# Kernel tuning notes

Hardware: AMD Instinct MI355X
Metric: run time of the kernel (lower is better)

## Reference

```python
import jax, jax.numpy as jnp
import numpy as np
import math

H = 1024          # hidden_size
NH = 16           # num heads
HD = H // NH      # head_dim = 64
ORDER = 2         # torsion_order
RANK = 64         # torsion_rank


def setup_inputs() -> dict:
    key = jax.random.key(0)
    ks = jax.random.split(key, 16)
    B, S = 2, 2048
    std = 0.02
    inp = {
        "hidden_states": jax.random.normal(ks[0], (B, S, H), jnp.float32),
        # projection weights stored [in, out] (equivalent to torch Linear W^T)
        "Wq": jax.random.normal(ks[1], (H, H), jnp.float32) * std,
        "bq": jnp.zeros((H,), jnp.float32),
        "Wk": jax.random.normal(ks[2], (H, H), jnp.float32) * std,
        "bk": jnp.zeros((H,), jnp.float32),
        "Wv": jax.random.normal(ks[3], (H, H), jnp.float32) * std,
        "bv": jnp.zeros((H,), jnp.float32),
        "Wo": jax.random.normal(ks[4], (H, H), jnp.float32) * std,
        "bo": jnp.zeros((H,), jnp.float32),
        "q_torsion_a": jax.random.normal(ks[5], (ORDER, H, RANK), jnp.float32) * 0.01,
        "q_torsion_b": jax.random.normal(ks[6], (ORDER, RANK, H), jnp.float32) * 0.01,
        "k_torsion_a": jax.random.normal(ks[7], (ORDER, H, RANK), jnp.float32) * 0.01,
        "k_torsion_b": jax.random.normal(ks[8], (ORDER, RANK, H), jnp.float32) * 0.01,
        "torsion_coupling": jnp.asarray(0.1, jnp.float32),
    }
    return inp


def _apply_torsion(x, ta, tb, coupling):
    # x: [B,S,H]; ta: [ORDER,H,R]; tb: [ORDER,R,H]
    corr = jnp.zeros_like(x)
    for n in range(ORDER):
        low = jnp.einsum('bsh,hr->bsr', x, ta[n])
        lin = jnp.einsum('bsr,rh->bsh', low, tb[n])
        phase = (2.0 * math.pi * (n + 1)) * lin
        corr = corr + jnp.sin(phase) * lin / (n + 1)
    return x + jax.nn.sigmoid(coupling) * corr


def reference(hidden_states, Wq, bq, Wk, bk, Wv, bv, Wo, bo,
              q_torsion_a, q_torsion_b, k_torsion_a, k_torsion_b,
              torsion_coupling):
    B, S, _ = hidden_states.shape
    q = hidden_states @ Wq + bq
    k = hidden_states @ Wk + bk
    v = hidden_states @ Wv + bv
    q = _apply_torsion(q, q_torsion_a, q_torsion_b, torsion_coupling)
    k = _apply_torsion(k, k_torsion_a, k_torsion_b, torsion_coupling)
    # [B, NH, S, HD]
    q = q.reshape(B, S, NH, HD).transpose(0, 2, 1, 3)
    k = k.reshape(B, S, NH, HD).transpose(0, 2, 1, 3)
    v = v.reshape(B, S, NH, HD).transpose(0, 2, 1, 3)
    scale = HD ** -0.5
    attn = jnp.einsum('bhqd,bhkd->bhqk', q, k) * scale
    attn = jax.nn.softmax(attn, axis=-1)
    out = jnp.einsum('bhqk,bhkd->bhqd', attn, v)
    out = out.transpose(0, 2, 1, 3).reshape(B, S, H)
    return out @ Wo + bo
```

## Files before the change

kernel.cpp:

```cpp
#include <hip/hip_runtime.h>
#include <hip/hip_bf16.h>
#include <cstdint>
#include <cstddef>

typedef __bf16 bf16_t;
typedef __bf16 bf16x8 __attribute__((ext_vector_type(8)));
typedef float f32x4 __attribute__((ext_vector_type(4)));

static __device__ __forceinline__ void st_out(float* p, float v) { *p = v; }
static __device__ __forceinline__ void st_out(bf16_t* p, float v) { *p = (bf16_t)v; }

static __device__ __forceinline__ void async_cp16(const bf16_t* g, bf16_t* l) {
  __builtin_amdgcn_global_load_lds(
      (const __attribute__((address_space(1))) void*)g,
      (__attribute__((address_space(3))) void*)l, 16, 0, 0);
}

__global__ __launch_bounds__(256) void prep(const float* __restrict__ hs, bf16_t* __restrict__ hsb,
                                            const float* __restrict__ Wq, const float* __restrict__ Wk,
                                            const float* __restrict__ Wv, const float* __restrict__ Wo,
                                            bf16_t* __restrict__ BtExt, bf16_t* __restrict__ WoT,
                                            bf16_t* __restrict__ Wqb, bf16_t* __restrict__ Wkb,
                                            const float* __restrict__ qta, const float* __restrict__ kta,
                                            bf16_t* __restrict__ qtaT, bf16_t* __restrict__ ktaT,
                                            const float* __restrict__ qtb, const float* __restrict__ ktb,
                                            bf16_t* __restrict__ qtbT, bf16_t* __restrict__ ktbT,
                                            const float* __restrict__ bq, const float* __restrict__ bk,
                                            const float* __restrict__ bv, float* __restrict__ biasN) {
  __shared__ float tile[32][33];
  const int bid = blockIdx.x, t = threadIdx.x;
  const int tx = t & 31, ty = t >> 5;

  if (bid < 2048) {
    int i = (bid * 256 + t) * 8;
    float4 a = *(const float4*)(hs + i);
    float4 b = *(const float4*)(hs + i + 4);
    union { bf16_t h[8]; uint4 u; } p;
    p.h[0] = (bf16_t)a.x; p.h[1] = (bf16_t)a.y; p.h[2] = (bf16_t)a.z; p.h[3] = (bf16_t)a.w;
    p.h[4] = (bf16_t)b.x; p.h[5] = (bf16_t)b.y; p.h[6] = (bf16_t)b.z; p.h[7] = (bf16_t)b.w;
    *(uint4*)(hsb + i) = p.u;
  } else if (bid < 6144) {
    int r = bid - 2048, z = r >> 10, r10 = r & 1023;
    int bx = (r10 & 31) * 32, by = (r10 >> 5) * 32;
    const float* src = z == 0 ? Wq : z == 1 ? Wk : z == 2 ? Wv : Wo;
    bf16_t* dst = z == 3 ? WoT : BtExt + (size_t)z * 1048576;
    bf16_t* sd = z == 0 ? Wqb : z == 1 ? Wkb : nullptr;
#pragma unroll
    for (int i = 0; i < 4; ++i) {
      float v = src[(size_t)(by + ty + i * 8) * 1024 + bx + tx];
      tile[ty + i * 8][tx] = v;
      if (sd) sd[(size_t)(by + ty + i * 8) * 1024 + bx + tx] = (bf16_t)v;
    }
    __syncthreads();
#pragma unroll
    for (int i = 0; i < 4; ++i)
      dst[(size_t)(bx + ty + i * 8) * 1024 + by + tx] = (bf16_t)tile[tx][ty + i * 8];
  } else if (bid < 6400) {
    int r = bid - 6144, z = r >> 6, r6 = r & 63;
    int bx = (r6 & 1) * 32, by = (r6 >> 1) * 32;
    const float* src = ((z >> 1) ? kta : qta) + (size_t)(z & 1) * 65536;
    bf16_t* dst = ((z >> 1) ? ktaT : qtaT) + (size_t)(z & 1) * 65536;
#pragma unroll
    for (int i = 0; i < 4; ++i)
      tile[ty + i * 8][tx] = src[(size_t)(by + ty + i * 8) * 64 + bx + tx];
    __syncthreads();
#pragma unroll
    for (int i = 0; i < 4; ++i)
      dst[(size_t)(bx + ty + i * 8) * 1024 + by + tx] = (bf16_t)tile[tx][ty + i * 8];
  } else if (bid < 6656) {
    int r = bid - 6400, z = r >> 6, r6 = r & 63;
    int bx = (r6 & 31) * 32, by = (r6 >> 5) * 32;
    const float* src = ((z >> 1) ? ktb : qtb) + (size_t)(z & 1) * 65536;
    bf16_t* dst = ((z >> 1) ? ktbT : qtbT) + (size_t)(z & 1) * 65536;
#pragma unroll
    for (int i = 0; i < 4; ++i)
      tile[ty + i * 8][tx] = src[(size_t)(by + ty + i * 8) * 1024 + bx + tx];
    __syncthreads();
#pragma unroll
    for (int i = 0; i < 4; ++i)
      dst[(size_t)(bx + ty + i * 8) * 64 + by + tx] = (bf16_t)tile[tx][ty + i * 8];
  } else if (bid < 6668) {
    int i = (bid - 6656) * 256 + t;
    biasN[i] = (i < 1024) ? bq[i] : (i < 2048 ? bk[i - 1024] : bv[i - 2048]);
  } else {
    int j = t;
    const float* b = (j < 128) ? bq : bk;
    const float* ta = ((j < 128) ? qta : kta) + (size_t)((j >> 6) & 1) * 65536;
    int rr = j & 63;
    float s = 0.f;
    for (int h = 0; h < 1024; ++h) s += b[h] * ta[(size_t)h * 64 + rr];
    biasN[3072 + j] = s;
  }
}

template <typename OutT>
static __device__ __forceinline__ void gemm_core_async(const bf16_t* __restrict__ A, int lda,
                                                       const bf16_t* __restrict__ Bt, int ldb,
                                                       OutT* __restrict__ C, int ldc,
                                                       const float* __restrict__ bias, int K,
                                                       int bx, int by) {
  __shared__ bf16_t As[128][32];
  __shared__ bf16_t Bs[128][32];
  const int m0 = by * 128, n0 = bx * 128;
  const int t = threadIdx.x, w = t >> 6, lane = t & 63;
  const int wm = (w >> 1) * 64, wn = (w & 1) * 64;
  const int quad = lane >> 4, l16 = lane & 15;
  const int sra = lane >> 2, sca = (lane & 3) * 8;
  const bf16_t* Ag0 = A + (size_t)(m0 + w * 16 + sra) * lda + sca;
  const bf16_t* Ag1 = A + (size_t)(m0 + 64 + w * 16 + sra) * lda + sca;
  const bf16_t* Bg0 = Bt + (size_t)(n0 + w * 16 + sra) * ldb + sca;
  const bf16_t* Bg1 = Bt + (size_t)(n0 + 64 + w * 16 + sra) * ldb + sca;
  bf16_t* la0 = &As[0][0] + w * 512;
  bf16_t* la1 = &As[0][0] + 2048 + w * 512;
  bf16_t* lb0 = &Bs[0][0] + w * 512;
  bf16_t* lb1 = &Bs[0][0] + 2048 + w * 512;

  f32x4 acc[4][4] = {};
  for (int k0 = 0; k0 < K; k0 += 32) {
    __syncthreads();
    async_cp16(Ag0 + k0, la0);
    async_cp16(Ag1 + k0, la1);
    async_cp16(Bg0 + k0, lb0);
    async_cp16(Bg1 + k0, lb1);
    __syncthreads();
    bf16x8 af[4], bfr[4];
#pragma unroll
    for (int i = 0; i < 4; ++i)
      af[i] = *(const bf16x8*)&As[wm + i * 16 + l16][quad * 8];
#pragma unroll
    for (int j = 0; j < 4; ++j)
      bfr[j] = *(const bf16x8*)&Bs[wn + j * 16 + l16][quad * 8];
#pragma unroll
    for (int i = 0; i < 4; ++i)
#pragma unroll
      for (int j = 0; j < 4; ++j)
        acc[i][j] = __builtin_amdgcn_mfma_f32_16x16x32_bf16(af[i], bfr[j], acc[i][j], 0, 0, 0);
  }
#pragma unroll
  for (int i = 0; i < 4; ++i) {
    int row = m0 + wm + i * 16 + quad * 4;
#pragma unroll
    for (int j = 0; j < 4; ++j) {
      int col = n0 + wn + j * 16 + l16;
      float bv = bias ? bias[col] : 0.f;
#pragma unroll
      for (int r = 0; r < 4; ++r)
        st_out(&C[(size_t)(row + r) * ldc + col], acc[i][j][r] + bv);
    }
  }
}

template <typename OutT>
static __device__ __forceinline__ void gemm_core_async64(const bf16_t* __restrict__ A, int lda,
                                                         const bf16_t* __restrict__ Bt, int ldb,
                                                         OutT* __restrict__ C, int ldc,
                                                         const float* __restrict__ bias, int K,
                                                         int bx, int by) {
  __shared__ bf16_t As[64][32];
  __shared__ bf16_t Bs[128][32];
  const int m0 = by * 64, n0 = bx * 128;
  const int t = threadIdx.x, w = t >> 6, lane = t & 63;
  const int wm = (w >> 1) * 32, wn = (w & 1) * 64;
  const int quad = lane >> 4, l16 = lane & 15;
  const int sra = lane >> 2, sca = (lane & 3) * 8;
  const bf16_t* Ag0 = A + (size_t)(m0 + w * 16 + sra) * lda + sca;
  const bf16_t* Bg0 = Bt + (size_t)(n0 + w * 16 + sra) * ldb + sca;
  const bf16_t* Bg1 = Bt + (size_t)(n0 + 64 + w * 16 + sra) * ldb + sca;
  bf16_t* la0 = &As[0][0] + w * 512;
  bf16_t* lb0 = &Bs[0][0] + w * 512;
  bf16_t* lb1 = &Bs[0][0] + 2048 + w * 512;

  f32x4 acc[2][4] = {};
  for (int k0 = 0; k0 < K; k0 += 32) {
    __syncthreads();
    async_cp16(Ag0 + k0, la0);
    async_cp16(Bg0 + k0, lb0);
    async_cp16(Bg1 + k0, lb1);
    __syncthreads();
    bf16x8 af[2], bfr[4];
#pragma unroll
    for (int i = 0; i < 2; ++i)
      af[i] = *(const bf16x8*)&As[wm + i * 16 + l16][quad * 8];
#pragma unroll
    for (int j = 0; j < 4; ++j)
      bfr[j] = *(const bf16x8*)&Bs[wn + j * 16 + l16][quad * 8];
#pragma unroll
    for (int i = 0; i < 2; ++i)
#pragma unroll
      for (int j = 0; j < 4; ++j)
        acc[i][j] = __builtin_amdgcn_mfma_f32_16x16x32_bf16(af[i], bfr[j], acc[i][j], 0, 0, 0);
  }
#pragma unroll
  for (int i = 0; i < 2; ++i) {
    int row = m0 + wm + i * 16 + quad * 4;
#pragma unroll
    for (int j = 0; j < 4; ++j) {
      int col = n0 + wn + j * 16 + l16;
      float bv = bias ? bias[col] : 0.f;
#pragma unroll
      for (int r = 0; r < 4; ++r)
        st_out(&C[(size_t)(row + r) * ldc + col], acc[i][j][r] + bv);
    }
  }
}

__global__ __launch_bounds__(256) void gemm_qkv(const bf16_t* __restrict__ A,
                                                const bf16_t* __restrict__ Bt,
                                                bf16_t* __restrict__ C,
                                                const float* __restrict__ biasN) {
  gemm_core_async<bf16_t>(A, 1024, Bt, 1024, C, 3328, biasN, 1024, blockIdx.x, blockIdx.y);
}

__global__ __launch_bounds__(256) void gemm_out(const bf16_t* __restrict__ A,
                                                const bf16_t* __restrict__ Bt,
                                                float* __restrict__ C,
                                                const float* __restrict__ bo) {
  gemm_core_async64<float>(A, 1024, Bt, 1024, C, 1024, bo, 1024, blockIdx.x, blockIdx.y);
}

__global__ __launch_bounds__(256) void gemm_wta(const bf16_t* __restrict__ qtaT,
                                                const bf16_t* __restrict__ ktaT,
                                                const bf16_t* __restrict__ Wqb,
                                                const bf16_t* __restrict__ Wkb,
                                                bf16_t* __restrict__ BtExt) {
  int z = blockIdx.z;
  gemm_core_async64<bf16_t>(z ? ktaT : qtaT, 1024, z ? Wkb : Wqb, 1024,
                            BtExt + (size_t)(3072 + z * 128) * 1024, 1024,
                            nullptr, 1024, blockIdx.x, blockIdx.y);
}

__global__ __launch_bounds__(256) void lin_torsion_fused(const bf16_t* __restrict__ qtbT,
                                                         const bf16_t* __restrict__ ktbT,
                                                         bf16_t* __restrict__ qkv,
                                                         const float* __restrict__ coupling) {
  __shared__ bf16_t As[128][136];
  __shared__ bf16_t Bs0[128][72];
  __shared__ bf16_t Bs1[128][72];
  const int z = blockIdx.z;
  const bf16_t* Low = qkv + 3072 + z * 128;
  const bf16_t* Tb = z ? ktbT : qtbT;
  bf16_t* X = qkv + z * 1024;

  const int m0 = blockIdx.y * 128, n0 = blockIdx.x * 128;
  const int t = threadIdx.x, w = t >> 6, lane = t & 63;
  const int wm = (w >> 1) * 64, wn = (w & 1) * 64;
  const int quad = lane >> 4, l16 = lane & 15;

  {
    const int sr = t >> 1, sc = (t & 1) * 64;
    const bf16_t* Ag = Low + (size_t)(m0 + sr) * 3328 + sc;
#pragma unroll
    for (int i = 0; i < 8; ++i)
      *(float4*)&As[sr][sc + 8 * i] = *(const float4*)(Ag + 8 * i);
    const int br = t >> 1, bc = (t & 1) * 32;
    const bf16_t* Bg0 = Tb + (size_t)(n0 + br) * 64 + bc;
    const bf16_t* Bg1 = Bg0 + 65536;
#pragma unroll
    for (int i = 0; i < 4; ++i) {
      *(float4*)&Bs0[br][bc + 8 * i] = *(const float4*)(Bg0 + 8 * i);
      *(float4*)&Bs1[br][bc + 8 * i] = *(const float4*)(Bg1 + 8 * i);
    }
  }
  __syncthreads();

  f32x4 acc0[4][4] = {}, acc1[4][4] = {};
#pragma unroll
  for (int ks = 0; ks < 2; ++ks) {
    bf16x8 a0[4], a1[4];
#pragma unroll
    for (int i = 0; i < 4; ++i) {
      a0[i] = *(const bf16x8*)&As[wm + i * 16 + l16][ks * 32 + quad * 8];
      a1[i] = *(const bf16x8*)&As[wm + i * 16 + l16][64 + ks * 32 + quad * 8];
    }
#pragma unroll
    for (int j = 0; j < 4; ++j) {
      bf16x8 b0 = *(const bf16x8*)&Bs0[wn + j * 16 + l16][ks * 32 + quad * 8];
      bf16x8 b1 = *(const bf16x8*)&Bs1[wn + j * 16 + l16][ks * 32 + quad * 8];
#pragma unroll
      for (int i = 0; i < 4; ++i) {
        acc0[i][j] = __builtin_amdgcn_mfma_f32_16x16x32_bf16(a0[i], b0, acc0[i][j], 0, 0, 0);
        acc1[i][j] = __builtin_amdgcn_mfma_f32_16x16x32_bf16(a1[i], b1, acc1[i][j], 0, 0, 0);
      }
    }
  }

  const float PI2 = 6.283185307179586f;
  const float sig = 1.f / (1.f + __expf(-coupling[0]));
  const float scale = z ? 1.f : 0.1803368801111204f;
#pragma unroll
  for (int i = 0; i < 4; ++i) {
#pragma unroll
    for (int j = 0; j < 4; ++j) {
#pragma unroll
      for (int r = 0; r < 4; ++r) {
        int row = m0 + wm + i * 16 + quad * 4 + r;
        int col = n0 + wn + j * 16 + l16;
        size_t idx = (size_t)row * 3328 + col;
        float l1 = acc0[i][j][r], l2 = acc1[i][j][r];
        float corr = __sinf(PI2 * l1) * l1 + __sinf(2.f * PI2 * l2) * l2 * 0.5f;
        X[idx] = (bf16_t)(((float)X[idx] + sig * corr) * scale);
      }
    }
  }
}

__global__ __launch_bounds__(256, 2) void flash_attn(const bf16_t* __restrict__ qkv,
                                                     bf16_t* __restrict__ aout) {
  constexpr int LD = 3328, SEQ = 2048;
  const int qb = blockIdx.x, bh = blockIdx.y;
  const int b = bh >> 4, h = bh & 15;
  const size_t base = (size_t)b * SEQ * LD + h * 64;
  const bf16_t* Qg = qkv + base;
  const bf16_t* Kg = qkv + base + 1024;
  const bf16_t* Vg = qkv + base + 2048;

  __shared__ __align__(16) unsigned char smem[29696];
  bf16_t(*VT)[136] = (bf16_t(*)[136])smem;
  float* LDSo = (float*)smem;
  float* Lred = (float*)(smem + 24576);
  float* invL = (float*)(smem + 28672);

  const int t = threadIdx.x, w = t >> 6, lane = t & 63;
  const int kw = w >> 1, qw = w & 1;
  const int quad = lane >> 4, l16 = lane & 15;
  const int q0 = qb * 128;

  bf16x8 qf[4][2];
  {
    const bf16_t* Qrow = Qg + (size_t)(q0 + qw * 64 + l16) * LD + quad * 8;
#pragma unroll
    for (int nf = 0; nf < 4; ++nf)
#pragma unroll
      for (int ks = 0; ks < 2; ++ks)
        qf[nf][ks] = *(const bf16x8*)(Qrow + (size_t)(nf * 16) * LD + ks * 32);
  }

  f32x4 o[4][4] = {};
  float l_part[4] = {0.f, 0.f, 0.f, 0.f};

  const int vg = t >> 3, vcb = (t & 7) * 8;
  const int colb = (((vg >> 3) << 5) | ((vg & 3) << 3) | (((vg >> 2) & 1) << 2)) ^ ((t & 7) << 3);
  const bf16_t* Vbase = Vg + (size_t)(vg * 4) * LD + vcb;
  const bf16_t* Krow = Kg + (size_t)(kw * 64 + l16) * LD + quad * 8;

  for (int k0 = 0; k0 < SEQ; k0 += 128) {
    __syncthreads();
    {
      const bf16_t* vsrc = Vbase + (size_t)k0 * LD;
      union { float4 f; bf16_t h[8]; } vr[4];
#pragma unroll
      for (int kk = 0; kk < 4; ++kk)
        vr[kk].f = *(const float4*)(vsrc + (size_t)kk * LD);
#pragma unroll
      for (int cc = 0; cc < 8; ++cc) {
        union { bf16_t h[4]; uint2 u; } pk;
#pragma unroll
        for (int kk = 0; kk < 4; ++kk) pk.h[kk] = vr[kk].h[cc];
        *(uint2*)&VT[vcb + cc][colb] = pk.u;
      }
    }
    bf16x8 kf[4][2];
#pragma unroll
    for (int jk = 0; jk < 4; ++jk)
#pragma unroll
      for (int ks = 0; ks < 2; ++ks)
        kf[jk][ks] = *(const bf16x8*)(Krow + (size_t)(k0 + jk * 16) * LD + ks * 32);
    __syncthreads();

    f32x4 st[4][4] = {};
#pragma unroll
    for (int ks = 0; ks < 2; ++ks)
#pragma unroll
      for (int jk = 0; jk < 4; ++jk)
#pragma unroll
        for (int nf = 0; nf < 4; ++nf)
          st[jk][nf] = __builtin_amdgcn_mfma_f32_16x16x32_bf16(kf[jk][ks], qf[nf][ks], st[jk][nf], 0, 0, 0);

    bf16x8 Pp[2][4];
#pragma unroll
    for (int g = 0; g < 2; ++g)
#pragma unroll
      for (int nf = 0; nf < 4; ++nf) {
        union { bf16_t h[8]; bf16x8 v; } ph;
#pragma unroll
        for (int b2 = 0; b2 < 2; ++b2)
#pragma unroll
          for (int r = 0; r < 4; ++r) {
            float p = exp2f(st[g * 2 + b2][nf][r]);
            l_part[nf] += p;
            ph.h[b2 * 4 + r] = (bf16_t)p;
          }
        Pp[g][nf] = ph.v;
      }

#pragma unroll
    for (int g = 0; g < 2; ++g) {
      bf16x8 vf[4];
#pragma unroll
      for (int jd = 0; jd < 4; ++jd) {
        int row = jd * 16 + l16;
        int col = (kw * 64 + g * 32 + quad * 8) ^ ((((row >> 3) & 7)) << 3);
        vf[jd] = *(const bf16x8*)&VT[row][col];
      }
#pragma unroll
      for (int jd = 0; jd < 4; ++jd)
#pragma unroll
        for (int nf = 0; nf < 4; ++nf)
          o[jd][nf] = __builtin_amdgcn_mfma_f32_16x16x32_bf16(vf[jd], Pp[g][nf], o[jd][nf], 0, 0, 0);
    }
  }

  __syncthreads();
#pragma unroll
  for (int nf = 0; nf < 4; ++nf)
    Lred[((kw * 2 + qw) * 4 + quad) * 64 + nf * 16 + l16] = l_part[nf];
  __syncthreads();
  if (t < 128) {
    int qw2 = t >> 6, ql = t & 63;
    float s = 0.f;
#pragma unroll
    for (int kw2 = 0; kw2 < 2; ++kw2)
#pragma unroll
      for (int qd = 0; qd < 4; ++qd)
        s += Lred[((kw2 * 2 + qw2) * 4 + qd) * 64 + ql];
    invL[t] = 1.f / s;
  }
  __syncthreads();

  const int rq = t >> 1, rc0 = (t & 1) * 8;
#pragma unroll
  for (int jd = 0; jd < 4; ++jd) {
#pragma unroll
    for (int nf = 0; nf < 4; ++nf)
      *(f32x4*)&LDSo[(size_t)(kw * 128 + qw * 64 + nf * 16 + l16) * 24 + quad * 4] = o[jd][nf];
    __syncthreads();
    f32x4 a0 = *(const f32x4*)&LDSo[(size_t)rq * 24 + rc0];
    f32x4 a1 = *(const f32x4*)&LDSo[(size_t)(128 + rq) * 24 + rc0];
    f32x4 b0 = *(const f32x4*)&LDSo[(size_t)rq * 24 + rc0 + 4];
    f32x4 b1 = *(const f32x4*)&LDSo[(size_t)(128 + rq) * 24 + rc0 + 4];
    float iv = invL[rq];
    union { bf16_t h[8]; uint4 u; } pk;
#pragma unroll
    for (int r = 0; r < 4; ++r) {
      pk.h[r] = (bf16_t)((a0[r] + a1[r]) * iv);
      pk.h[4 + r] = (bf16_t)((b0[r] + b1[r]) * iv);
    }
    *(uint4*)&aout[(size_t)(b * SEQ + q0 + rq) * 1024 + h * 64 + jd * 16 + rc0] = pk.u;
    if (jd < 3) __syncthreads();
  }
}

extern "C" void kernel_launch(void* const* d_in, const int* in_sizes, int n_in,
                              void* d_out, int out_size, void* d_ws, size_t ws_size,
                              hipStream_t stream) {
  const float* hs   = (const float*)d_in[0];
  const float* Wq   = (const float*)d_in[1];
  const float* bq   = (const float*)d_in[2];
  const float* Wk   = (const float*)d_in[3];
  const float* bk   = (const float*)d_in[4];
  const float* Wv   = (const float*)d_in[5];
  const float* bv   = (const float*)d_in[6];
  const float* Wo   = (const float*)d_in[7];
  const float* bo   = (const float*)d_in[8];
  const float* qta  = (const float*)d_in[9];
  const float* qtb  = (const float*)d_in[10];
  const float* kta  = (const float*)d_in[11];
  const float* ktb  = (const float*)d_in[12];
  const float* coup = (const float*)d_in[13];
  float* out = (float*)d_out;

  uint8_t* ws = (uint8_t*)d_ws;
  bf16_t* hsb   = (bf16_t*)(ws);
  bf16_t* aout  = (bf16_t*)(ws);
  bf16_t* BtExt = (bf16_t*)(ws + 8388608);
  bf16_t* WoT   = (bf16_t*)(ws + 16777216);
  float*  biasN = (float*)(ws + 18874368);
  bf16_t* qkv   = (bf16_t*)(ws + 18890752);
  bf16_t* Wqb   = (bf16_t*)(ws + 46153728);
  bf16_t* Wkb   = (bf16_t*)(ws + 48250880);
  bf16_t* qtaT  = (bf16_t*)(ws + 50348032);
  bf16_t* ktaT  = (bf16_t*)(ws + 50610176);
  bf16_t* qtbT  = (bf16_t*)(ws + 50872320);
  bf16_t* ktbT  = (bf16_t*)(ws + 51134464);

  dim3 b256(256);

  prep<<<6669, b256, 0, stream>>>(hs, hsb, Wq, Wk, Wv, Wo, BtExt, WoT, Wqb, Wkb,
                                  qta, kta, qtaT, ktaT, qtb, ktb, qtbT, ktbT,
                                  bq, bk, bv, biasN);
  gemm_wta<<<dim3(8, 2, 2), b256, 0, stream>>>(qtaT, ktaT, Wqb, Wkb, BtExt);
  gemm_qkv<<<dim3(26, 32), b256, 0, stream>>>(hsb, BtExt, qkv, biasN);
  lin_torsion_fused<<<dim3(8, 32, 2), b256, 0, stream>>>(qtbT, ktbT, qkv, coup);
  flash_attn<<<dim3(16, 32), b256, 0, stream>>>(qkv, aout);
  gemm_out<<<dim3(8, 64), b256, 0, stream>>>(aout, WoT, out, bo);
}
```

Baseline: 290.4 us.

## Double-buffer V tile in LDS and prefetch next K/V in flash attention

```diff
diff --git a/kernel.cpp b/kernel.cpp
--- a/kernel.cpp
+++ b/kernel.cpp
@@ -314,8 +314,9 @@
   const bf16_t* Kg = qkv + base + 1024;
   const bf16_t* Vg = qkv + base + 2048;
 
-  __shared__ __align__(16) unsigned char smem[29696];
-  bf16_t(*VT)[136] = (bf16_t(*)[136])smem;
+  __shared__ __align__(16) unsigned char smem[34816];
+  bf16_t(*VT0)[136] = (bf16_t(*)[136])smem;
+  bf16_t(*VT1)[136] = (bf16_t(*)[136])(smem + 17408);
   float* LDSo = (float*)smem;
   float* Lred = (float*)(smem + 24576);
   float* invL = (float*)(smem + 28672);
@@ -343,31 +344,35 @@
   const bf16_t* Vbase = Vg + (size_t)(vg * 4) * LD + vcb;
   const bf16_t* Krow = Kg + (size_t)(kw * 64 + l16) * LD + quad * 8;
 
+  float4 vr[4];
+  bf16x8 kf[4][2];
+
+#pragma unroll
+  for (int kk = 0; kk < 4; ++kk)
+    vr[kk] = *(const float4*)(Vbase + (size_t)kk * LD);
+#pragma unroll
+  for (int cc = 0; cc < 8; ++cc) {
+    union { bf16_t h[4]; uint2 u; } pk;
+#pragma unroll
+    for (int kk = 0; kk < 4; ++kk) pk.h[kk] = ((const bf16_t*)&vr[kk])[cc];
+    *(uint2*)&VT0[vcb + cc][colb] = pk.u;
+  }
+#pragma unroll
+  for (int kk = 0; kk < 4; ++kk)
+    vr[kk] = *(const float4*)(Vbase + (size_t)(128 + kk) * LD);
+#pragma unroll
+  for (int jk = 0; jk < 4; ++jk)
+#pragma unroll
+    for (int ks = 0; ks < 2; ++ks)
+      kf[jk][ks] = *(const bf16x8*)(Krow + (size_t)(jk * 16) * LD + ks * 32);
+  __syncthreads();
+
   for (int k0 = 0; k0 < SEQ; k0 += 128) {
-    __syncthreads();
-    {
-      const bf16_t* vsrc = Vbase + (size_t)k0 * LD;
-      union { float4 f; bf16_t h[8]; } vr[4];
-#pragma unroll
-      for (int kk = 0; kk < 4; ++kk)
-        vr[kk].f = *(const float4*)(vsrc + (size_t)kk * LD);
-#pragma unroll
-      for (int cc = 0; cc < 8; ++cc) {
-        union { bf16_t h[4]; uint2 u; } pk;
-#pragma unroll
-        for (int kk = 0; kk < 4; ++kk) pk.h[kk] = vr[kk].h[cc];
-        *(uint2*)&VT[vcb + cc][colb] = pk.u;
-      }
-    }
-    bf16x8 kf[4][2];
-#pragma unroll
-    for (int jk = 0; jk < 4; ++jk)
-#pragma unroll
-      for (int ks = 0; ks < 2; ++ks)
-        kf[jk][ks] = *(const bf16x8*)(Krow + (size_t)(k0 + jk * 16) * LD + ks * 32);
-    __syncthreads();
+    bf16_t(*VTc)[136] = ((k0 >> 7) & 1) ? VT1 : VT0;
+    bf16_t(*VTn)[136] = ((k0 >> 7) & 1) ? VT0 : VT1;
 
     f32x4 st[4][4] = {};
+    __builtin_amdgcn_s_setprio(1);
 #pragma unroll
     for (int ks = 0; ks < 2; ++ks)
 #pragma unroll
@@ -375,24 +380,45 @@
 #pragma unroll
         for (int nf = 0; nf < 4; ++nf)
           st[jk][nf] = __builtin_amdgcn_mfma_f32_16x16x32_bf16(kf[jk][ks], qf[nf][ks], st[jk][nf], 0, 0, 0);
+    __builtin_amdgcn_s_setprio(0);
 
     bf16x8 Pp[2][4];
 #pragma unroll
     for (int g = 0; g < 2; ++g)
 #pragma unroll
       for (int nf = 0; nf < 4; ++nf) {
-        union { bf16_t h[8]; bf16x8 v; } ph;
+        union { bf16_t hh[8]; bf16x8 v; } ph;
 #pragma unroll
         for (int b2 = 0; b2 < 2; ++b2)
 #pragma unroll
           for (int r = 0; r < 4; ++r) {
             float p = exp2f(st[g * 2 + b2][nf][r]);
             l_part[nf] += p;
-            ph.h[b2 * 4 + r] = (bf16_t)p;
+            ph.hh[b2 * 4 + r] = (bf16_t)p;
           }
         Pp[g][nf] = ph.v;
       }
 
+    if (k0 + 128 < SEQ) {
+#pragma unroll
+      for (int cc = 0; cc < 8; ++cc) {
+        union { bf16_t h[4]; uint2 u; } pk;
+#pragma unroll
+        for (int kk = 0; kk < 4; ++kk) pk.h[kk] = ((const bf16_t*)&vr[kk])[cc];
+        *(uint2*)&VTn[vcb + cc][colb] = pk.u;
+      }
+      if (k0 + 256 < SEQ) {
+#pragma unroll
+        for (int kk = 0; kk < 4; ++kk)
+          vr[kk] = *(const float4*)(Vbase + (size_t)(k0 + 256 + kk) * LD);
+      }
+#pragma unroll
+      for (int jk = 0; jk < 4; ++jk)
+#pragma unroll
+        for (int ks = 0; ks < 2; ++ks)
+          kf[jk][ks] = *(const bf16x8*)(Krow + (size_t)(k0 + 128 + jk * 16) * LD + ks * 32);
+    }
+
 #pragma unroll
     for (int g = 0; g < 2; ++g) {
       bf16x8 vf[4];
@@ -400,17 +426,20 @@
       for (int jd = 0; jd < 4; ++jd) {
         int row = jd * 16 + l16;
         int col = (kw * 64 + g * 32 + quad * 8) ^ ((((row >> 3) & 7)) << 3);
-        vf[jd] = *(const bf16x8*)&VT[row][col];
+        vf[jd] = *(const bf16x8*)&VTc[row][col];
       }
+      __builtin_amdgcn_s_setprio(1);
 #pragma unroll
       for (int jd = 0; jd < 4; ++jd)
 #pragma unroll
         for (int nf = 0; nf < 4; ++nf)
           o[jd][nf] = __builtin_amdgcn_mfma_f32_16x16x32_bf16(vf[jd], Pp[g][nf], o[jd][nf], 0, 0, 0);
-    }
-  }
-
-  __syncthreads();
+      __builtin_amdgcn_s_setprio(0);
+    }
+
+    __syncthreads();
+  }
+
 #pragma unroll
   for (int nf = 0; nf < 4; ++nf)
     Lred[((kw * 2 + qw) * 4 + quad) * 64 + nf * 16 + l16] = l_part[nf];
```

After: 301.6 us. 1.04x slower.
